# Performance work log

Measured on AMD Instinct MI355X. Metric: run time of the kernel, lower is better.

Reference implementation:

```python
import jax, jax.numpy as jnp
import numpy as np

STEP = 2
NEG = -1.0e10  # matches masked_fill_(-10000000000.0)


def leaky_relu(x):
    # nn.LeakyReLU(0.2)
    return jnp.where(x >= 0, x, 0.2 * x)


def setup_inputs() -> dict:
    key = jax.random.key(0)
    k1, k2, k3, k4 = jax.random.split(key, 4)
    B, E, N, H = 16, 1024, 1024, 128
    nodes_hidden = jax.random.normal(k1, (B, N, H), dtype=jnp.float32)
    # sparse-ish binary hyperedge incidence matrix (batch, edge_num, node_num)
    hn_adj = jax.random.bernoulli(k2, 0.1, (B, E, N)).astype(jnp.float32)
    # Linear(H+1, 1, bias=False) weights for q1 / q2, flattened to (H+1,)
    w1 = jax.random.normal(k3, (H + 1,), dtype=jnp.float32) / np.sqrt(H + 1).astype(np.float32)
    w2 = jax.random.normal(k4, (H + 1,), dtype=jnp.float32) / np.sqrt(H + 1).astype(np.float32)
    return {"nodes_hidden": nodes_hidden, "hn_adj": hn_adj, "w1": w1, "w2": w2}


def reference(nodes_hidden, hn_adj, w1, w2):
    # Dropout is inference-mode identity.
    H = nodes_hidden.shape[-1]
    # edge init: mean of incident node features
    deg = jnp.sum(hn_adj, axis=-1, keepdims=True)            # (B,E,1)
    deg = jnp.where(deg == 0.0, 1.0, deg)
    edge = jnp.matmul(hn_adj, nodes_hidden) / deg            # (B,E,H)
    nodes = nodes_hidden
    for _ in range(STEP):
        # q1(concat(edge*node, adj)) == (edge*node)@w1[:H] + adj*w1[H]
        # fused rank-1 score: never materialize (B,E,N,H)
        alpha = leaky_relu(
            jnp.einsum("bed,bnd,d->ben", edge, nodes, w1[:H]) + hn_adj * w1[H]
        )                                                     # (B,E,N)
        alpha = jnp.where(hn_adj == 0, NEG, alpha)
        alpha = jax.nn.softmax(alpha, axis=-1)
        edge = jnp.einsum("ben,bnd->bed", alpha, nodes)       # new edge hidden
        adj_t = jnp.swapaxes(hn_adj, 1, 2)                    # (B,N,E)
        beta = leaky_relu(
            jnp.einsum("bed,bnd,d->bne", edge, nodes, w2[:H]) + adj_t * w2[H]
        )                                                     # (B,N,E)
        beta = jnp.where(adj_t == 0, NEG, beta)
        beta = jax.nn.softmax(beta, axis=-1)
        nodes = jnp.einsum("bne,bed->bnd", beta, edge)        # new node hidden
    return (nodes, edge)
```

## Files before the change

### kernel.cpp

```cpp
#include <hip/hip_runtime.h>
#include <cstdint>
#include <cstddef>

#define B_ 16
#define E_ 1024
#define N_ 1024
#define H_ 128
#define CAP 192
#define NC 32
#define EC 32

typedef unsigned short u16;

#define UPK2(u, flo, fhi) \
    flo = __uint_as_float((u) << 16); fhi = __uint_as_float((u) & 0xffff0000u)

__device__ __forceinline__ u16 f2bf(float f) {
    unsigned u = __float_as_uint(f);
    return (u16)((u + 0x7fffu + ((u >> 16) & 1u)) >> 16);
}

__device__ __forceinline__ float wave_sum64(float v) {
    v += __shfl_xor(v, 32);
    v += __shfl_xor(v, 16);
    v += __shfl_xor(v, 8);
    v += __shfl_xor(v, 4);
    v += __shfl_xor(v, 2);
    v += __shfl_xor(v, 1);
    return v;
}

__global__ void build_rows(const float* __restrict__ adj,
                           u16* __restrict__ idx, int* __restrict__ cnt_out) {
    int be = blockIdx.x;
    const float* row = adj + (size_t)be * N_;
    __shared__ int wcnt[4];
    __shared__ int base;
    int tid = threadIdx.x, lane = tid & 63, wv = tid >> 6;
    if (tid == 0) base = 0;
    __syncthreads();
    for (int c0 = 0; c0 < N_; c0 += 256) {
        float v = row[c0 + tid];
        unsigned long long m = __ballot(v != 0.0f);
        if (lane == 0) wcnt[wv] = __popcll(m);
        __syncthreads();
        int pos = base;
        for (int w = 0; w < wv; ++w) pos += wcnt[w];
        pos += __popcll(m & ((1ull << lane) - 1ull));
        if (v != 0.0f && pos < CAP)
            idx[(size_t)be * CAP + pos] = (u16)(c0 + tid);
        __syncthreads();
        if (tid == 0) base += wcnt[0] + wcnt[1] + wcnt[2] + wcnt[3];
        __syncthreads();
    }
    if (tid == 0) cnt_out[be] = base < CAP ? base : CAP;
}

__global__ void col_count(const float* __restrict__ adj, int* __restrict__ cnt_chunk) {
    int blk = blockIdx.x;
    int ng = blk & 3;
    int c  = (blk >> 2) & (NC - 1);
    int b  = blk >> 7;
    int n = (ng << 8) + threadIdx.x;
    const float* base = adj + ((size_t)(b * E_ + c * EC)) * N_ + n;
    int cc = 0;
#pragma unroll 8
    for (int e = 0; e < EC; ++e)
        cc += (base[(size_t)e * N_] != 0.0f);
    cnt_chunk[(size_t)(b * NC + c) * N_ + n] = cc;
}

__global__ void col_prefix(const int* __restrict__ cnt_chunk,
                           int* __restrict__ off_chunk, int* __restrict__ cnt_out) {
    int idx = blockIdx.x * 256 + threadIdx.x;
    int b = idx >> 10, n = idx & 1023;
    int run = 0;
    for (int c = 0; c < NC; ++c) {
        size_t p = (size_t)(b * NC + c) * N_ + n;
        off_chunk[p] = run;
        run += cnt_chunk[p];
    }
    cnt_out[idx] = run < CAP ? run : CAP;
}

__global__ void col_place(const float* __restrict__ adj,
                          const int* __restrict__ off_chunk, u16* __restrict__ idx) {
    int blk = blockIdx.x;
    int ng = blk & 3;
    int c  = (blk >> 2) & (NC - 1);
    int b  = blk >> 7;
    int n = (ng << 8) + threadIdx.x;
    const float* base = adj + ((size_t)(b * E_ + c * EC)) * N_ + n;
    int pos = off_chunk[(size_t)(b * NC + c) * N_ + n];
    u16* lst = idx + ((size_t)b * N_ + n) * CAP;
    for (int e = 0; e < EC; ++e) {
        if (base[(size_t)e * N_] != 0.0f) {
            if (pos < CAP) lst[pos] = (u16)(c * EC + e);
            ++pos;
        }
    }
}

__global__ void to_bf16(const float* __restrict__ in, u16* __restrict__ out) {
    int i = blockIdx.x * 256 + threadIdx.x;
    float4 v = ((const float4*)in)[i];
    ushort4 r;
    r.x = f2bf(v.x); r.y = f2bf(v.y); r.z = f2bf(v.z); r.w = f2bf(v.w);
    ((ushort4*)out)[i] = r;
}

__global__ void __launch_bounds__(256, 4)
edge_init(const u16* __restrict__ nodes_bf,
          const u16* __restrict__ ridx, const int* __restrict__ rcnt,
          float* __restrict__ edge) {
    int x = blockIdx.x;
    int xcd = x & 7;
    int j = x >> 3;
    int b = xcd + ((j >> 8) << 3);
    int rg = (j & 255) << 2;
    int tid = threadIdx.x, lane = tid & 63, wv = tid >> 6;
    int be = (b << 10) + rg + wv;
    __shared__ u16 sidx[4][CAP];
    int cnt = rcnt[be];
    for (int i = lane; i < cnt; i += 64) sidx[wv][i] = ridx[(size_t)be * CAP + i];

    int esub = lane >> 3, dsub = lane & 7;
    const uint4* kb4 = (const uint4*)(nodes_bf + (size_t)b * N_ * H_);
    float4 a0 = make_float4(0.f, 0.f, 0.f, 0.f);
    float4 a1 = a0, a2 = a0, a3 = a0;

    unsigned ro = (unsigned)((esub < cnt) ? sidx[wv][esub] : 0) * 16 + (dsub << 1);
    uint4 g0 = kb4[ro];
    uint4 g1 = kb4[ro + 1];

    for (int i0 = 0; i0 < cnt; i0 += 8) {
        int inx = i0 + 8 + esub;
        unsigned rn = (unsigned)((inx < cnt) ? sidx[wv][inx] : 0) * 16 + (dsub << 1);
        uint4 n0 = kb4[rn];
        uint4 n1 = kb4[rn + 1];
        int i = i0 + esub;
        float f0, f1, f2, f3, f4, f5, f6, f7;
        float f8, f9, f10, f11, f12, f13, f14, f15;
        UPK2(g0.x, f0, f1);   UPK2(g0.y, f2, f3);
        UPK2(g0.z, f4, f5);   UPK2(g0.w, f6, f7);
        UPK2(g1.x, f8, f9);   UPK2(g1.y, f10, f11);
        UPK2(g1.z, f12, f13); UPK2(g1.w, f14, f15);
        float ww = (i < cnt) ? 1.0f : 0.f;
        a0.x = fmaf(ww, f0, a0.x);  a0.y = fmaf(ww, f1, a0.y);
        a0.z = fmaf(ww, f2, a0.z);  a0.w = fmaf(ww, f3, a0.w);
        a1.x = fmaf(ww, f4, a1.x);  a1.y = fmaf(ww, f5, a1.y);
        a1.z = fmaf(ww, f6, a1.z);  a1.w = fmaf(ww, f7, a1.w);
        a2.x = fmaf(ww, f8, a2.x);  a2.y = fmaf(ww, f9, a2.y);
        a2.z = fmaf(ww, f10, a2.z); a2.w = fmaf(ww, f11, a2.w);
        a3.x = fmaf(ww, f12, a3.x); a3.y = fmaf(ww, f13, a3.y);
        a3.z = fmaf(ww, f14, a3.z); a3.w = fmaf(ww, f15, a3.w);
        g0 = n0; g1 = n1;
    }

#define RED3(f) f += __shfl_xor(f, 8); f += __shfl_xor(f, 16); f += __shfl_xor(f, 32)
    RED3(a0.x); RED3(a0.y); RED3(a0.z); RED3(a0.w);
    RED3(a1.x); RED3(a1.y); RED3(a1.z); RED3(a1.w);
    RED3(a2.x); RED3(a2.y); RED3(a2.z); RED3(a2.w);
    RED3(a3.x); RED3(a3.y); RED3(a3.z); RED3(a3.w);
#undef RED3
    if (esub == 0) {
        float inv = 1.0f / (float)(cnt > 0 ? cnt : 1);
        a0.x *= inv; a0.y *= inv; a0.z *= inv; a0.w *= inv;
        a1.x *= inv; a1.y *= inv; a1.z *= inv; a1.w *= inv;
        a2.x *= inv; a2.y *= inv; a2.z *= inv; a2.w *= inv;
        a3.x *= inv; a3.y *= inv; a3.z *= inv; a3.w *= inv;
        float4* op = (float4*)edge + (size_t)be * 32 + (dsub << 2);
        op[0] = a0; op[1] = a1; op[2] = a2; op[3] = a3;
    }
}

__global__ void __launch_bounds__(256, 4)
attn_gather(const float* __restrict__ qsrc,
            const u16* __restrict__ kv_bf,
            const float* __restrict__ w,
            const u16* __restrict__ lidx, const int* __restrict__ lcnt,
            float* __restrict__ out, u16* __restrict__ out_bf, int wbf) {
    int x = blockIdx.x;
    int xcd = x & 7;
    int j = x >> 3;
    int b = xcd + ((j >> 8) << 3);
    int rg = (j & 255) << 2;
    int tid = threadIdx.x, lane = tid & 63, wv = tid >> 6;
    int br = (b << 10) + rg + wv;
    __shared__ u16 sidx[4][CAP];
    int cnt = lcnt[br];
    for (int i = lane; i < cnt; i += 64) sidx[wv][i] = lidx[(size_t)br * CAP + i];

    int esub = lane >> 3, dsub = lane & 7;
    const float4* qp = (const float4*)(qsrc + (size_t)br * H_);
    const float4* wp = (const float4*)w;
    float4 qr0, qr1, qr2, qr3;
    {
        float4 q0 = qp[(dsub << 2) + 0], w0 = wp[(dsub << 2) + 0];
        float4 q1 = qp[(dsub << 2) + 1], w1 = wp[(dsub << 2) + 1];
        float4 q2 = qp[(dsub << 2) + 2], w2 = wp[(dsub << 2) + 2];
        float4 q3 = qp[(dsub << 2) + 3], w3 = wp[(dsub << 2) + 3];
        const float L2E = 1.44269504f;
        qr0.x = q0.x * w0.x * L2E; qr0.y = q0.y * w0.y * L2E;
        qr0.z = q0.z * w0.z * L2E; qr0.w = q0.w * w0.w * L2E;
        qr1.x = q1.x * w1.x * L2E; qr1.y = q1.y * w1.y * L2E;
        qr1.z = q1.z * w1.z * L2E; qr1.w = q1.w * w1.w * L2E;
        qr2.x = q2.x * w2.x * L2E; qr2.y = q2.y * w2.y * L2E;
        qr2.z = q2.z * w2.z * L2E; qr2.w = q2.w * w2.w * L2E;
        qr3.x = q3.x * w3.x * L2E; qr3.y = q3.y * w3.y * L2E;
        qr3.z = q3.z * w3.z * L2E; qr3.w = q3.w * w3.w * L2E;
    }
    float wb = w[H_] * 1.44269504f;
    const uint4* kb4 = (const uint4*)(kv_bf + (size_t)b * 1024 * H_);

    float4 a0 = make_float4(0.f, 0.f, 0.f, 0.f);
    float4 a1 = a0, a2 = a0, a3 = a0;
    float dpart = 0.f;

    unsigned ro = (unsigned)((esub < cnt) ? sidx[wv][esub] : 0) * 16 + (dsub << 1);
    uint4 g0 = kb4[ro];
    uint4 g1 = kb4[ro + 1];

    for (int i0 = 0; i0 < cnt; i0 += 8) {
        int inx = i0 + 8 + esub;
        unsigned rn = (unsigned)((inx < cnt) ? sidx[wv][inx] : 0) * 16 + (dsub << 1);
        uint4 n0 = kb4[rn];
        uint4 n1 = kb4[rn + 1];
        int i = i0 + esub;
        float f0, f1, f2, f3, f4, f5, f6, f7;
        float f8, f9, f10, f11, f12, f13, f14, f15;
        UPK2(g0.x, f0, f1);   UPK2(g0.y, f2, f3);
        UPK2(g0.z, f4, f5);   UPK2(g0.w, f6, f7);
        UPK2(g1.x, f8, f9);   UPK2(g1.y, f10, f11);
        UPK2(g1.z, f12, f13); UPK2(g1.w, f14, f15);
        float dA = 0.f, dB = 0.f;
        dA = fmaf(f0, qr0.x, dA);  dB = fmaf(f1, qr0.y, dB);
        dA = fmaf(f2, qr0.z, dA);  dB = fmaf(f3, qr0.w, dB);
        dA = fmaf(f4, qr1.x, dA);  dB = fmaf(f5, qr1.y, dB);
        dA = fmaf(f6, qr1.z, dA);  dB = fmaf(f7, qr1.w, dB);
        dA = fmaf(f8, qr2.x, dA);  dB = fmaf(f9, qr2.y, dB);
        dA = fmaf(f10, qr2.z, dA); dB = fmaf(f11, qr2.w, dB);
        dA = fmaf(f12, qr3.x, dA); dB = fmaf(f13, qr3.y, dB);
        dA = fmaf(f14, qr3.z, dA); dB = fmaf(f15, qr3.w, dB);
        float d = dA + dB;
        d += __shfl_xor(d, 1);
        d += __shfl_xor(d, 2);
        d += __shfl_xor(d, 4);
        float p = d + wb;
        p = p >= 0.f ? p : 0.2f * p;
        float ww = (i < cnt) ? exp2f(p) : 0.f;
        dpart += ww;
        a0.x = fmaf(ww, f0, a0.x);  a0.y = fmaf(ww, f1, a0.y);
        a0.z = fmaf(ww, f2, a0.z);  a0.w = fmaf(ww, f3, a0.w);
        a1.x = fmaf(ww, f4, a1.x);  a1.y = fmaf(ww, f5, a1.y);
        a1.z = fmaf(ww, f6, a1.z);  a1.w = fmaf(ww, f7, a1.w);
        a2.x = fmaf(ww, f8, a2.x);  a2.y = fmaf(ww, f9, a2.y);
        a2.z = fmaf(ww, f10, a2.z); a2.w = fmaf(ww, f11, a2.w);
        a3.x = fmaf(ww, f12, a3.x); a3.y = fmaf(ww, f13, a3.y);
        a3.z = fmaf(ww, f14, a3.z); a3.w = fmaf(ww, f15, a3.w);
        g0 = n0; g1 = n1;
    }

#define RED3(f) f += __shfl_xor(f, 8); f += __shfl_xor(f, 16); f += __shfl_xor(f, 32)
    RED3(a0.x); RED3(a0.y); RED3(a0.z); RED3(a0.w);
    RED3(a1.x); RED3(a1.y); RED3(a1.z); RED3(a1.w);
    RED3(a2.x); RED3(a2.y); RED3(a2.z); RED3(a2.w);
    RED3(a3.x); RED3(a3.y); RED3(a3.z); RED3(a3.w);
#undef RED3
    float denom = wave_sum64(dpart) * 0.125f;
    float rden = denom > 0.f ? 1.0f / denom : 0.f;

    if (esub == 0) {
        a0.x *= rden; a0.y *= rden; a0.z *= rden; a0.w *= rden;
        a1.x *= rden; a1.y *= rden; a1.z *= rden; a1.w *= rden;
        a2.x *= rden; a2.y *= rden; a2.z *= rden; a2.w *= rden;
        a3.x *= rden; a3.y *= rden; a3.z *= rden; a3.w *= rden;
        float4* op = (float4*)out + (size_t)br * 32 + (dsub << 2);
        op[0] = a0; op[1] = a1; op[2] = a2; op[3] = a3;
        if (wbf) {
            ushort4* hp = (ushort4*)out_bf + (size_t)br * 32 + (dsub << 2);
            ushort4 h0, h1, h2, h3;
            h0.x = f2bf(a0.x); h0.y = f2bf(a0.y); h0.z = f2bf(a0.z); h0.w = f2bf(a0.w);
            h1.x = f2bf(a1.x); h1.y = f2bf(a1.y); h1.z = f2bf(a1.z); h1.w = f2bf(a1.w);
            h2.x = f2bf(a2.x); h2.y = f2bf(a2.y); h2.z = f2bf(a2.z); h2.w = f2bf(a2.w);
            h3.x = f2bf(a3.x); h3.y = f2bf(a3.y); h3.z = f2bf(a3.z); h3.w = f2bf(a3.w);
            hp[0] = h0; hp[1] = h1; hp[2] = h2; hp[3] = h3;
        }
    }
}

extern "C" void kernel_launch(void* const* d_in, const int* in_sizes, int n_in,
                              void* d_out, int out_size, void* d_ws, size_t ws_size,
                              hipStream_t stream) {
    const float* nodes_in = (const float*)d_in[0];
    const float* adj      = (const float*)d_in[1];
    const float* w1       = (const float*)d_in[2];
    const float* w2       = (const float*)d_in[3];

    char* ws = (char*)d_ws;
    size_t off = 0;
    u16* row_idx = (u16*)(ws + off); off += (size_t)B_ * E_ * CAP * sizeof(u16);
    u16* col_idx = (u16*)(ws + off); off += (size_t)B_ * N_ * CAP * sizeof(u16);
    int* row_cnt = (int*)(ws + off); off += (size_t)B_ * E_ * sizeof(int);
    int* col_cnt = (int*)(ws + off); off += (size_t)B_ * N_ * sizeof(int);
    int* cnt_chunk = (int*)(ws + off); off += (size_t)B_ * NC * N_ * sizeof(int);
    int* off_chunk = (int*)(ws + off); off += (size_t)B_ * NC * N_ * sizeof(int);
    u16* nodes_bf = (u16*)(ws + off); off += (size_t)B_ * N_ * H_ * sizeof(u16);
    u16* edge_bf  = (u16*)(ws + off); off += (size_t)B_ * E_ * H_ * sizeof(u16);

    float* out_nodes = (float*)d_out;
    float* out_edge  = out_nodes + (size_t)B_ * N_ * H_;

    build_rows<<<dim3(B_ * E_), dim3(256), 0, stream>>>(adj, row_idx, row_cnt);
    col_count <<<dim3(B_ * NC * 4), dim3(256), 0, stream>>>(adj, cnt_chunk);
    col_prefix<<<dim3(B_ * N_ / 256), dim3(256), 0, stream>>>(cnt_chunk, off_chunk, col_cnt);
    col_place <<<dim3(B_ * NC * 4), dim3(256), 0, stream>>>(adj, off_chunk, col_idx);
    to_bf16   <<<dim3(B_ * N_ * H_ / 1024), dim3(256), 0, stream>>>(nodes_in, nodes_bf);
    edge_init <<<dim3(B_ * E_ / 4), dim3(256), 0, stream>>>(nodes_bf, row_idx, row_cnt, out_edge);

    const float* ncur = nodes_in;
    for (int s = 0; s < 2; ++s) {
        attn_gather<<<dim3(B_ * E_ / 4), dim3(256), 0, stream>>>(
            out_edge, nodes_bf, w1, row_idx, row_cnt, out_edge, edge_bf, 1);
        attn_gather<<<dim3(B_ * N_ / 4), dim3(256), 0, stream>>>(
            ncur, edge_bf, w2, col_idx, col_cnt, out_nodes, nodes_bf, s == 0 ? 1 : 0);
        ncur = out_nodes;
    }
}
```

Measured before the change: 232.8 us.

## Read adjacency once into bitmask, build row/col lists from bits; raise occupancy

Reads the float adjacency matrix once and packs it into 64-bit ballot bitmasks. The row index lists, column counts and column placement are then built from the compact bitmask instead of re-reading the 64 MB float matrix three times. Row list building now uses one wave per row, with a wave prefix scan replacing the block-wide syncthreads loop. Launch bounds for edge_init and attn_gather are also raised to 8 blocks per CU, which may force register spills.

```diff
diff --git a/kernel.cpp b/kernel.cpp
--- a/kernel.cpp
+++ b/kernel.cpp
@@ -9,8 +9,10 @@
 #define CAP 192
 #define NC 32
 #define EC 32
+#define NW 16
 
 typedef unsigned short u16;
+typedef unsigned long long u64;
 
 #define UPK2(u, flo, fhi) \
     flo = __uint_as_float((u) << 16); fhi = __uint_as_float((u) & 0xffff0000u)
@@ -30,43 +32,57 @@
     return v;
 }
 
-__global__ void build_rows(const float* __restrict__ adj,
-                           u16* __restrict__ idx, int* __restrict__ cnt_out) {
+__global__ void adj_to_bits(const float* __restrict__ adj, u64* __restrict__ bits) {
     int be = blockIdx.x;
     const float* row = adj + (size_t)be * N_;
-    __shared__ int wcnt[4];
-    __shared__ int base;
     int tid = threadIdx.x, lane = tid & 63, wv = tid >> 6;
-    if (tid == 0) base = 0;
-    __syncthreads();
     for (int c0 = 0; c0 < N_; c0 += 256) {
         float v = row[c0 + tid];
-        unsigned long long m = __ballot(v != 0.0f);
-        if (lane == 0) wcnt[wv] = __popcll(m);
-        __syncthreads();
-        int pos = base;
-        for (int w = 0; w < wv; ++w) pos += wcnt[w];
-        pos += __popcll(m & ((1ull << lane) - 1ull));
-        if (v != 0.0f && pos < CAP)
-            idx[(size_t)be * CAP + pos] = (u16)(c0 + tid);
-        __syncthreads();
-        if (tid == 0) base += wcnt[0] + wcnt[1] + wcnt[2] + wcnt[3];
-        __syncthreads();
-    }
-    if (tid == 0) cnt_out[be] = base < CAP ? base : CAP;
-}
-
-__global__ void col_count(const float* __restrict__ adj, int* __restrict__ cnt_chunk) {
+        u64 m = __ballot(v != 0.0f);
+        if (lane == 0) bits[(size_t)be * NW + (c0 >> 6) + wv] = m;
+    }
+}
+
+__global__ void rows_from_bits(const u64* __restrict__ bits,
+                               u16* __restrict__ idx, int* __restrict__ cnt_out) {
+    int x = blockIdx.x;
+    int tid = threadIdx.x, lane = tid & 63, wv = tid >> 6;
+    int be = (x << 2) + wv;
+    const u64* wds = bits + (size_t)be * NW;
+    u64 m = (lane < NW) ? wds[lane] : 0ull;
+    int pc = __popcll(m);
+    int inc = pc;
+#pragma unroll
+    for (int o = 1; o < 64; o <<= 1) {
+        int t = __shfl_up(inc, o);
+        if (lane >= o) inc += t;
+    }
+    int excl = inc - pc;
+    int total = __shfl(inc, 63);
+    u16* lst = idx + (size_t)be * CAP;
+    int pos = excl;
+    u64 mm = m;
+    while (mm) {
+        int bno = __ffsll(mm) - 1;
+        if (pos < CAP) lst[pos] = (u16)((lane << 6) + bno);
+        ++pos;
+        mm &= mm - 1;
+    }
+    if (lane == 0) cnt_out[be] = total < CAP ? total : CAP;
+}
+
+__global__ void col_count_bits(const u64* __restrict__ bits, int* __restrict__ cnt_chunk) {
     int blk = blockIdx.x;
     int ng = blk & 3;
     int c  = (blk >> 2) & (NC - 1);
     int b  = blk >> 7;
     int n = (ng << 8) + threadIdx.x;
-    const float* base = adj + ((size_t)(b * E_ + c * EC)) * N_ + n;
+    const u64* base = bits + ((size_t)(b * E_ + c * EC)) * NW + (n >> 6);
+    u64 sel = 1ull << (n & 63);
     int cc = 0;
 #pragma unroll 8
     for (int e = 0; e < EC; ++e)
-        cc += (base[(size_t)e * N_] != 0.0f);
+        cc += (base[(size_t)e * NW] & sel) ? 1 : 0;
     cnt_chunk[(size_t)(b * NC + c) * N_ + n] = cc;
 }
 
@@ -83,18 +99,19 @@
     cnt_out[idx] = run < CAP ? run : CAP;
 }
 
-__global__ void col_place(const float* __restrict__ adj,
-                          const int* __restrict__ off_chunk, u16* __restrict__ idx) {
+__global__ void col_place_bits(const u64* __restrict__ bits,
+                               const int* __restrict__ off_chunk, u16* __restrict__ idx) {
     int blk = blockIdx.x;
     int ng = blk & 3;
     int c  = (blk >> 2) & (NC - 1);
     int b  = blk >> 7;
     int n = (ng << 8) + threadIdx.x;
-    const float* base = adj + ((size_t)(b * E_ + c * EC)) * N_ + n;
+    const u64* base = bits + ((size_t)(b * E_ + c * EC)) * NW + (n >> 6);
+    u64 sel = 1ull << (n & 63);
     int pos = off_chunk[(size_t)(b * NC + c) * N_ + n];
     u16* lst = idx + ((size_t)b * N_ + n) * CAP;
     for (int e = 0; e < EC; ++e) {
-        if (base[(size_t)e * N_] != 0.0f) {
+        if (base[(size_t)e * NW] & sel) {
             if (pos < CAP) lst[pos] = (u16)(c * EC + e);
             ++pos;
         }
@@ -109,7 +126,7 @@
     ((ushort4*)out)[i] = r;
 }
 
-__global__ void __launch_bounds__(256, 4)
+__global__ void __launch_bounds__(256, 8)
 edge_init(const u16* __restrict__ nodes_bf,
           const u16* __restrict__ ridx, const int* __restrict__ rcnt,
           float* __restrict__ edge) {
@@ -174,7 +191,7 @@
     }
 }
 
-__global__ void __launch_bounds__(256, 4)
+__global__ void __launch_bounds__(256, 8)
 attn_gather(const float* __restrict__ qsrc,
             const u16* __restrict__ kv_bf,
             const float* __restrict__ w,
@@ -307,16 +324,18 @@
     int* off_chunk = (int*)(ws + off); off += (size_t)B_ * NC * N_ * sizeof(int);
     u16* nodes_bf = (u16*)(ws + off); off += (size_t)B_ * N_ * H_ * sizeof(u16);
     u16* edge_bf  = (u16*)(ws + off); off += (size_t)B_ * E_ * H_ * sizeof(u16);
+    u64* bits     = (u64*)(ws + off); off += (size_t)B_ * E_ * NW * sizeof(u64);
 
     float* out_nodes = (float*)d_out;
     float* out_edge  = out_nodes + (size_t)B_ * N_ * H_;
 
-    build_rows<<<dim3(B_ * E_), dim3(256), 0, stream>>>(adj, row_idx, row_cnt);
-    col_count <<<dim3(B_ * NC * 4), dim3(256), 0, stream>>>(adj, cnt_chunk);
-    col_prefix<<<dim3(B_ * N_ / 256), dim3(256), 0, stream>>>(cnt_chunk, off_chunk, col_cnt);
-    col_place <<<dim3(B_ * NC * 4), dim3(256), 0, stream>>>(adj, off_chunk, col_idx);
-    to_bf16   <<<dim3(B_ * N_ * H_ / 1024), dim3(256), 0, stream>>>(nodes_in, nodes_bf);
-    edge_init <<<dim3(B_ * E_ / 4), dim3(256), 0, stream>>>(nodes_bf, row_idx, row_cnt, out_edge);
+    adj_to_bits   <<<dim3(B_ * E_), dim3(256), 0, stream>>>(adj, bits);
+    rows_from_bits<<<dim3(B_ * E_ / 4), dim3(256), 0, stream>>>(bits, row_idx, row_cnt);
+    col_count_bits<<<dim3(B_ * NC * 4), dim3(256), 0, stream>>>(bits, cnt_chunk);
+    col_prefix    <<<dim3(B_ * N_ / 256), dim3(256), 0, stream>>>(cnt_chunk, off_chunk, col_cnt);
+    col_place_bits<<<dim3(B_ * NC * 4), dim3(256), 0, stream>>>(bits, off_chunk, col_idx);
+    to_bf16       <<<dim3(B_ * N_ * H_ / 1024), dim3(256), 0, stream>>>(nodes_in, nodes_bf);
+    edge_init     <<<dim3(B_ * E_ / 4), dim3(256), 0, stream>>>(nodes_bf, row_idx, row_cnt, out_edge);
 
     const float* ncur = nodes_in;
     for (int s = 0; s < 2; ++s) {
```

New measurement: 232.5 us. Within noise of the previous version (-0.1%).
